# Performance work log

Measured on AMD Instinct MI355X. Metric: run time of the kernel, lower is better.

The kernel has to match this reference:

```python
import jax, jax.numpy as jnp
import numpy as np

L, B, E = 2048, 4, 1024
H = 8
D1 = 2048          # expand_ratio * E, multiple of H
HD = D1 // H       # head dim 256
MAX_L = 2048
EPS = 1e-8


def setup_inputs() -> dict:
    key = jax.random.key(0)
    ks = jax.random.split(key, 9)
    std = 0.02
    return {
        "x": jax.random.normal(ks[0], (L, B, E), jnp.float32),
        "Wu": jax.random.normal(ks[1], (D1, E), jnp.float32) * std,
        "bu": jax.random.normal(ks[2], (D1,), jnp.float32) * std,
        "Wv": jax.random.normal(ks[3], (D1, E), jnp.float32) * std,
        "bv": jax.random.normal(ks[4], (D1,), jnp.float32) * std,
        "Wo": jax.random.normal(ks[5], (E, D1), jnp.float32) * std,
        "bo": jax.random.normal(ks[6], (E,), jnp.float32) * std,
        "zero": jax.random.normal(ks[7], (H, 1), jnp.float32) * 0.1,   # Toeplitz coef, offset 0
        "pos": jax.random.normal(ks[8], (H, MAX_L - 1), jnp.float32) * 0.1,  # offsets 1..n-1
    }


def _simple_rmsnorm(x):
    d = x.shape[-1]
    rms = jnp.linalg.norm(x, axis=-1, keepdims=True) * (d ** -0.5)
    return x / (rms + EPS)


def _toeplitz_causal_fft(v, zero, pos):
    # v: (b, h, n, hd); causal Toeplitz mixing along n via FFT long conv
    n = v.shape[-2]
    coef = jnp.concatenate([zero, pos[:, : n - 1]], axis=-1)  # (h, n)
    m = 2 * n
    cf = jnp.fft.rfft(coef, m, axis=-1)                  # (h, m//2+1)
    vf = jnp.fft.rfft(v, m, axis=-2)                     # (b, h, m//2+1, hd)
    out = jnp.fft.irfft(cf[None, :, :, None] * vf, m, axis=-2)
    return out[:, :, :n, :]


def reference(x, Wu, bu, Wv, bv, Wo, bo, zero, pos):
    # x: (n, b, e) fairseq layout
    n, b, e = x.shape
    shortcut = x
    xn = _simple_rmsnorm(x)                               # pre_norm (SimpleRMSNorm, no params)
    u = jax.nn.silu(jnp.einsum('nbe,de->nbd', xn, Wu) + bu)   # (n,b,d1)
    v = jax.nn.silu(jnp.einsum('nbe,de->nbd', xn, Wv) + bv)   # (n,b,d1)
    # 'n b (h d) -> b h n d'
    vh = v.transpose(1, 0, 2).reshape(b, n, H, HD).transpose(0, 2, 1, 3)
    oh = _toeplitz_causal_fft(vh, zero, pos)              # (b,h,n,hd)
    o = oh.transpose(0, 2, 1, 3).reshape(b, n, D1).transpose(1, 0, 2)  # (n,b,d1)
    o = u * o                                             # gating
    out = jnp.einsum('nbd,ed->nbe', o, Wo) + bo + shortcut
    return out
```

## Files before the change

### kernel.cpp

```cpp
#include <hip/hip_runtime.h>
#include <cstdint>
#include <cstddef>

#define LQ   2048
#define BQ   4
#define EQ   1024
#define HQ   8
#define D1Q  2048
#define HDQ  256
#define NBQ  (LQ*BQ)

typedef __bf16 bf16_t;
typedef __bf16 bf16x8 __attribute__((ext_vector_type(8)));
typedef __bf16 bf16x4 __attribute__((ext_vector_type(4)));
typedef float  f32x4  __attribute__((ext_vector_type(4)));

#define GAS1(p) ((const __attribute__((address_space(1))) void*)(p))
#define LAS3(p) ((__attribute__((address_space(3))) void*)(p))


__global__ __launch_bounds__(256) void convert_kernel(
    const float* __restrict__ Wu, const float* __restrict__ Wv,
    const float* __restrict__ Wo,
    bf16_t* __restrict__ Wub, bf16_t* __restrict__ Wvb,
    bf16_t* __restrict__ Wob)
{
    const size_t i = (size_t)blockIdx.x * 256 + threadIdx.x;
    if (i < (size_t)D1Q * EQ) {
        Wub[i] = (bf16_t)Wu[i];
        Wvb[i] = (bf16_t)Wv[i];
        Wob[i] = (bf16_t)Wo[i];
    }
}

__global__ __launch_bounds__(256) void build_toep_tiles(
    const float* __restrict__ zero, const float* __restrict__ pos,
    bf16_t* __restrict__ Atiles)
{
    const int q = blockIdx.x;
    const int h = blockIdx.y;
    const int doff = (q - 3) * 32;
    const int tid = threadIdx.x;
    bf16_t* dst = Atiles + ((size_t)h * 64 + q) * (128 * 32);
    const int e0 = tid * 16;
    const int r = e0 >> 5;
    const int cbase = e0 & 31;
    bf16_t vals[16];
    #pragma unroll
    for (int j = 0; j < 16; ++j) {
        const int d = doff + r - (cbase + j);
        float v = 0.f;
        if (d == 0) v = zero[h];
        else if (d > 0) v = pos[(size_t)h * (LQ - 1) + d - 1];
        vals[j] = (bf16_t)v;
    }
    *(bf16x8*)(dst + e0)     = *(bf16x8*)(vals);
    *(bf16x8*)(dst + e0 + 8) = *(bf16x8*)(vals + 8);
}

__global__ __launch_bounds__(256) void rmsnorm_kernel(
    const float* __restrict__ x, bf16_t* __restrict__ xn)
{
    const int row = blockIdx.x;
    const int tid = threadIdx.x;
    const float4 v = ((const float4*)(x + (size_t)row * EQ))[tid];
    float ss = v.x*v.x + v.y*v.y + v.z*v.z + v.w*v.w;
    #pragma unroll
    for (int m = 32; m >= 1; m >>= 1) ss += __shfl_xor(ss, m, 64);
    __shared__ float red[4];
    const int wid = tid >> 6, lane = tid & 63;
    if (lane == 0) red[wid] = ss;
    __syncthreads();
    const float tot = red[0] + red[1] + red[2] + red[3];
    const float inv = 1.f / (sqrtf(tot * (1.f / EQ)) + 1e-8f);
    bf16x4 o;
    o[0] = (bf16_t)(v.x * inv); o[1] = (bf16_t)(v.y * inv);
    o[2] = (bf16_t)(v.z * inv); o[3] = (bf16_t)(v.w * inv);
    *(bf16x4*)(xn + (size_t)row * EQ + tid * 4) = o;
}

__global__ __launch_bounds__(256) void transpose_v(
    const bf16_t* __restrict__ V, bf16_t* __restrict__ VT)
{
    __shared__ bf16_t tile[64][65];
    const int bh = blockIdx.z;
    const int b = bh >> 3, h = bh & 7;
    const int s0 = blockIdx.x * 64, hd0 = blockIdx.y * 64;
    const int tid = threadIdx.x;
    #pragma unroll
    for (int p = 0; p < 16; ++p) {
        const int idx = p * 256 + tid;
        const int i = idx >> 6;
        const int j = idx & 63;
        tile[i][j] = V[((size_t)(s0 + i) * BQ + b) * D1Q + h * HDQ + hd0 + j];
    }
    __syncthreads();
    #pragma unroll
    for (int p = 0; p < 16; ++p) {
        const int idx = p * 256 + tid;
        const int i = idx >> 6;
        const int j = idx & 63;
        VT[((size_t)bh * HDQ + hd0 + i) * LQ + s0 + j] = tile[j][i];
    }
}


template<int NREP, int MODE>
__global__ __launch_bounds__(512, 1) void gemm8p(
    const bf16_t* __restrict__ A, const bf16_t* __restrict__ Bm,
    int K, int N,
    const float* __restrict__ bias, const float* __restrict__ res,
    bf16_t* __restrict__ Cb, float* __restrict__ Cf)
{
    constexpr int LB      = NREP / 2;
    constexpr int BSTRIDE = 16384 + NREP * 4096;
    __shared__ alignas(16) char smem[3 * BSTRIDE];

    const int tid  = threadIdx.x;
    const int wid  = tid >> 6;
    const int lane = tid & 63;
    const int frow = lane & 15;
    const int c    = lane >> 4;
    const int m0 = blockIdx.y * 256;
    const int n0 = blockIdx.x * (NREP * 64);
    const int wrm = (wid >> 2) * 128;
    const int wrn = (wid & 3) * (NREP * 16);

    const int Ra = wrm + frow;
    const int ga = (Ra ^ (Ra >> 2)) & 3;
    const int offA = Ra * 64 + ((c ^ ga) << 4);
    const int Rb = wrn + frow;
    const int gb = (Rb ^ (Rb >> 2)) & 3;
    const int offB = 16384 + Rb * 64 + ((c ^ gb) << 4);

    const int sr   = tid >> 2;
    const int slot = tid & 3;
    const int gs   = (sr ^ (sr >> 2)) & 3;
    const size_t lda = (size_t)K * 2;
    const char* srcA  = (const char*)A  + (size_t)(m0 + sr) * lda + ((slot ^ gs) << 4);
    const char* srcA2 = srcA + 128 * lda;
    const char* srcB  = (const char*)Bm + (size_t)(n0 + sr) * lda + ((slot ^ gs) << 4);
    const char* srcB2 = srcB + 128 * lda;

    auto STAGE_A = [&](int buf, int kt) {
        char* d = smem + buf * BSTRIDE + wid * 1024;
        __builtin_amdgcn_global_load_lds(GAS1(srcA  + (size_t)kt * 64), LAS3(d), 16, 0, 0);
        __builtin_amdgcn_global_load_lds(GAS1(srcA2 + (size_t)kt * 64), LAS3(d + 8192), 16, 0, 0);
    };
    auto STAGE_B = [&](int buf, int kt) {
        char* d = smem + buf * BSTRIDE + 16384 + wid * 1024;
        __builtin_amdgcn_global_load_lds(GAS1(srcB  + (size_t)kt * 64), LAS3(d), 16, 0, 0);
        if constexpr (LB == 2)
            __builtin_amdgcn_global_load_lds(GAS1(srcB2 + (size_t)kt * 64), LAS3(d + 8192), 16, 0, 0);
    };

    f32x4 acc[8][NREP];
    #pragma unroll
    for (int i = 0; i < 8; ++i)
        #pragma unroll
        for (int j = 0; j < NREP; ++j) acc[i][j] = (f32x4){0.f, 0.f, 0.f, 0.f};

    const int NT = K >> 5;

    STAGE_A(0, 0); STAGE_B(0, 0);
    STAGE_A(1, 1); STAGE_B(1, 1);
    if constexpr (LB == 2) asm volatile("s_waitcnt vmcnt(4)" ::: "memory");
    else                   asm volatile("s_waitcnt vmcnt(3)" ::: "memory");
    __builtin_amdgcn_s_barrier();

    int buf = 0;
    for (int kq = 0; kq < NT; ++kq) {
        const char* base = smem + buf * BSTRIDE;
        int pbuf = buf + 2; if (pbuf >= 3) pbuf -= 3;
        const bool pf = (kq < NT - 2);

        bf16x8 av[4], bv[NREP];
        #pragma unroll
        for (int i = 0; i < 4; ++i)
            av[i] = *(const bf16x8*)(base + offA + i * 1024);
        #pragma unroll
        for (int i = 0; i < NREP; ++i)
            bv[i] = *(const bf16x8*)(base + offB + i * 1024);
        if (pf) STAGE_A(pbuf, kq + 2);
        __builtin_amdgcn_s_barrier();
        __builtin_amdgcn_s_setprio(1);
        #pragma unroll
        for (int mi = 0; mi < 4; ++mi)
            #pragma unroll
            for (int ni = 0; ni < NREP; ++ni)
                acc[mi][ni] = __builtin_amdgcn_mfma_f32_16x16x32_bf16(
                    av[mi], bv[ni], acc[mi][ni], 0, 0, 0);
        __builtin_amdgcn_s_setprio(0);
        __builtin_amdgcn_sched_barrier(0);
        __builtin_amdgcn_s_barrier();

        #pragma unroll
        for (int i = 0; i < 4; ++i)
            av[i] = *(const bf16x8*)(base + offA + (4 + i) * 1024);
        if (pf) STAGE_B(pbuf, kq + 2);
        __builtin_amdgcn_s_barrier();
        __builtin_amdgcn_s_setprio(1);
        #pragma unroll
        for (int mi = 0; mi < 4; ++mi)
            #pragma unroll
            for (int ni = 0; ni < NREP; ++ni)
                acc[4 + mi][ni] = __builtin_amdgcn_mfma_f32_16x16x32_bf16(
                    av[mi], bv[ni], acc[4 + mi][ni], 0, 0, 0);
        __builtin_amdgcn_s_setprio(0);
        __builtin_amdgcn_sched_barrier(0);

        if (kq < NT - 1) {
            if (kq <= NT - 3) {
                if constexpr (LB == 2) asm volatile("s_waitcnt vmcnt(4)" ::: "memory");
                else                   asm volatile("s_waitcnt vmcnt(3)" ::: "memory");
            } else {
                asm volatile("s_waitcnt vmcnt(0)" ::: "memory");
            }
            __builtin_amdgcn_s_barrier();
        }
        buf = (buf == 2) ? 0 : buf + 1;
    }

    const int fq = (lane >> 4) * 4;
    #pragma unroll
    for (int mi = 0; mi < 8; ++mi) {
        #pragma unroll
        for (int ni = 0; ni < NREP; ++ni) {
            const int gn = n0 + wrn + ni * 16 + frow;
            #pragma unroll
            for (int j = 0; j < 4; ++j) {
                const int gm = m0 + wrm + mi * 16 + fq + j;
                float v = acc[mi][ni][j];
                if constexpr (MODE == 0) {
                    v += bias[gn];
                    v = v / (1.f + __expf(-v));
                    Cb[(size_t)gm * N + gn] = (bf16_t)v;
                } else {
                    v += bias[gn] + res[(size_t)gm * N + gn];
                    Cf[(size_t)gm * N + gn] = v;
                }
            }
        }
    }
}

__global__ __launch_bounds__(256) void gemm_toep(
    const bf16_t* __restrict__ VT, const bf16_t* __restrict__ Atiles,
    const bf16_t* __restrict__ U, bf16_t* __restrict__ O)
{
    constexpr int BM = 128, BN = 128, BK = 32;
    __shared__ alignas(16) bf16_t As[BM * BK];
    __shared__ alignas(16) bf16_t Bs[BN * BK];

    const int bid   = blockIdx.x;
    const int m_blk = 15 - (bid >> 6);
    const int sub   = bid & 63;
    const int bh    = sub >> 1;
    const int n0    = (sub & 1) * BN;
    const int b = bh >> 3, h = bh & 7;
    const int m0 = m_blk * BM;

    const int tid  = threadIdx.x;
    const int wid  = tid >> 6;
    const int lane = tid & 63;
    const int wr = (wid >> 1) * 64;
    const int wc = (wid & 1) * 64;

    f32x4 acc[4][4];
    #pragma unroll
    for (int i = 0; i < 4; ++i)
        #pragma unroll
        for (int j = 0; j < 4; ++j) acc[i][j] = (f32x4){0.f, 0.f, 0.f, 0.f};

    const int off0 = wid * 1024 + lane * 16;
    const int off1 = off0 + 4096;
    const int r0 = off0 >> 6, c0 = off0 & 63;
    const int r1 = off1 >> 6, c1 = off1 & 63;
    const char* Bb = (const char*)(VT + ((size_t)bh * HDQ + n0) * LQ);
    const size_t ldb = (size_t)LQ * 2;
    const char* Ah = (const char*)(Atiles + (size_t)h * 64 * 4096);

    const int frow = lane & 15;
    const int fk   = (lane >> 4) * 8;
    const int nk   = 4 * m_blk + 4;

    for (int kq = 0; kq < nk; ++kq) {
        const int k0 = kq * 32;
        const char* At = Ah + (size_t)((m_blk << 2) + 3 - kq) * 8192;
        __builtin_amdgcn_global_load_lds(GAS1(At + off0),
                                         LAS3((char*)As + wid * 1024), 16, 0, 0);
        __builtin_amdgcn_global_load_lds(GAS1(At + off1),
                                         LAS3((char*)As + 4096 + wid * 1024), 16, 0, 0);
        __builtin_amdgcn_global_load_lds(GAS1(Bb + (size_t)r0 * ldb + (size_t)k0 * 2 + c0),
                                         LAS3((char*)Bs + wid * 1024), 16, 0, 0);
        __builtin_amdgcn_global_load_lds(GAS1(Bb + (size_t)r1 * ldb + (size_t)k0 * 2 + c1),
                                         LAS3((char*)Bs + 4096 + wid * 1024), 16, 0, 0);
        __syncthreads();

        bf16x8 af[4], bfv[4];
        #pragma unroll
        for (int i = 0; i < 4; ++i) {
            af[i]  = *(const bf16x8*)(As + (wr + i * 16 + frow) * BK + fk);
            bfv[i] = *(const bf16x8*)(Bs + (wc + i * 16 + frow) * BK + fk);
        }
        #pragma unroll
        for (int mi = 0; mi < 4; ++mi)
            #pragma unroll
            for (int ni = 0; ni < 4; ++ni)
                acc[mi][ni] = __builtin_amdgcn_mfma_f32_16x16x32_bf16(
                    af[mi], bfv[ni], acc[mi][ni], 0, 0, 0);
        __syncthreads();
    }

    const int fq = (lane >> 4) * 4;
    #pragma unroll
    for (int mi = 0; mi < 4; ++mi) {
        #pragma unroll
        for (int ni = 0; ni < 4; ++ni) {
            const int hd = n0 + wc + ni * 16 + frow;
            #pragma unroll
            for (int j = 0; j < 4; ++j) {
                const int t = m0 + wr + mi * 16 + fq + j;
                const size_t idx = ((size_t)t * BQ + b) * D1Q + h * HDQ + hd;
                const float uval = (float)U[idx];
                O[idx] = (bf16_t)(uval * acc[mi][ni][j]);
            }
        }
    }
}


extern "C" void kernel_launch(void* const* d_in, const int* in_sizes, int n_in,
                              void* d_out, int out_size, void* d_ws, size_t ws_size,
                              hipStream_t stream)
{
    const float* x    = (const float*)d_in[0];
    const float* Wu   = (const float*)d_in[1];
    const float* bu   = (const float*)d_in[2];
    const float* Wv   = (const float*)d_in[3];
    const float* bv   = (const float*)d_in[4];
    const float* Wo   = (const float*)d_in[5];
    const float* bo   = (const float*)d_in[6];
    const float* zero = (const float*)d_in[7];
    const float* pos  = (const float*)d_in[8];
    float* out = (float*)d_out;

    char* ws = (char*)d_ws;
    size_t off = 0;
    auto alloc = [&](size_t bytes) {
        char* p = ws + off;
        off += (bytes + 255) & ~(size_t)255;
        return p;
    };
    bf16_t* xn     = (bf16_t*)alloc((size_t)NBQ * EQ * 2);
    bf16_t* Wub    = (bf16_t*)alloc((size_t)D1Q * EQ * 2);
    bf16_t* Wvb    = (bf16_t*)alloc((size_t)D1Q * EQ * 2);
    bf16_t* Wob    = (bf16_t*)alloc((size_t)EQ * D1Q * 2);
    bf16_t* Atiles = (bf16_t*)alloc((size_t)HQ * 64 * 4096 * 2);
    bf16_t* Ub     = (bf16_t*)alloc((size_t)NBQ * D1Q * 2);
    bf16_t* Vb     = (bf16_t*)alloc((size_t)NBQ * D1Q * 2);
    bf16_t* VTb    = (bf16_t*)alloc((size_t)NBQ * D1Q * 2);
    bf16_t* Ob     = (bf16_t*)alloc((size_t)NBQ * D1Q * 2);

    convert_kernel<<<8192, 256, 0, stream>>>(Wu, Wv, Wo, Wub, Wvb, Wob);
    build_toep_tiles<<<dim3(64, 8), 256, 0, stream>>>(zero, pos, Atiles);
    rmsnorm_kernel<<<NBQ, 256, 0, stream>>>(x, xn);

    dim3 g1(D1Q / 256, NBQ / 256);
    gemm8p<4, 0><<<g1, 512, 0, stream>>>(xn, Wub, EQ, D1Q, bu, nullptr, Ub, nullptr);
    gemm8p<4, 0><<<g1, 512, 0, stream>>>(xn, Wvb, EQ, D1Q, bv, nullptr, Vb, nullptr);

    transpose_v<<<dim3(LQ / 64, HDQ / 64, BQ * HQ), 256, 0, stream>>>(Vb, VTb);

    gemm_toep<<<1024, 256, 0, stream>>>(VTb, Atiles, Ub, Ob);

    dim3 g2(EQ / 128, NBQ / 256);
    gemm8p<2, 2><<<g2, 512, 0, stream>>>(Ob, Wob, D1Q, EQ, bo, x, nullptr, out);
}
```

Measured before the change: 236.5 us.

## Fuse V transpose into GEMM epilogue, batch Toeplitz over B, remap workgroups

```diff
diff --git a/kernel.cpp b/kernel.cpp
--- a/kernel.cpp
+++ b/kernel.cpp
@@ -79,31 +79,6 @@
     *(bf16x4*)(xn + (size_t)row * EQ + tid * 4) = o;
 }
 
-__global__ __launch_bounds__(256) void transpose_v(
-    const bf16_t* __restrict__ V, bf16_t* __restrict__ VT)
-{
-    __shared__ bf16_t tile[64][65];
-    const int bh = blockIdx.z;
-    const int b = bh >> 3, h = bh & 7;
-    const int s0 = blockIdx.x * 64, hd0 = blockIdx.y * 64;
-    const int tid = threadIdx.x;
-    #pragma unroll
-    for (int p = 0; p < 16; ++p) {
-        const int idx = p * 256 + tid;
-        const int i = idx >> 6;
-        const int j = idx & 63;
-        tile[i][j] = V[((size_t)(s0 + i) * BQ + b) * D1Q + h * HDQ + hd0 + j];
-    }
-    __syncthreads();
-    #pragma unroll
-    for (int p = 0; p < 16; ++p) {
-        const int idx = p * 256 + tid;
-        const int i = idx >> 6;
-        const int j = idx & 63;
-        VT[((size_t)bh * HDQ + hd0 + i) * LQ + s0 + j] = tile[j][i];
-    }
-}
-
 
 template<int NREP, int MODE>
 __global__ __launch_bounds__(512, 1) void gemm8p(
@@ -116,13 +91,20 @@
     constexpr int BSTRIDE = 16384 + NREP * 4096;
     __shared__ alignas(16) char smem[3 * BSTRIDE];
 
+    const int nwg   = gridDim.x * gridDim.y;
+    const int bid   = blockIdx.y * gridDim.x + blockIdx.x;
+    const int chunk = nwg >> 3;
+    const int sb    = (bid & 7) * chunk + (bid >> 3);
+    const int bx    = sb % gridDim.x;
+    const int by    = sb / gridDim.x;
+
     const int tid  = threadIdx.x;
     const int wid  = tid >> 6;
     const int lane = tid & 63;
     const int frow = lane & 15;
     const int c    = lane >> 4;
-    const int m0 = blockIdx.y * 256;
-    const int n0 = blockIdx.x * (NREP * 64);
+    const int m0 = by * 256;
+    const int n0 = bx * (NREP * 64);
     const int wrm = (wid >> 2) * 128;
     const int wrn = (wid & 3) * (NREP * 16);
 
@@ -221,7 +203,7 @@
         buf = (buf == 2) ? 0 : buf + 1;
     }
 
-    const int fq = (lane >> 4) * 4;
+    const int fq = c * 4;
     #pragma unroll
     for (int mi = 0; mi < 8; ++mi) {
         #pragma unroll
@@ -235,6 +217,12 @@
                     v += bias[gn];
                     v = v / (1.f + __expf(-v));
                     Cb[(size_t)gm * N + gn] = (bf16_t)v;
+                } else if constexpr (MODE == 1) {
+                    v += bias[gn];
+                    v = v / (1.f + __expf(-v));
+                    const int t = gm >> 2, b2 = gm & 3;
+                    const int hh = gn >> 8, hd = gn & 255;
+                    Cb[(((size_t)hh * 4 + b2) * 256 + hd) * LQ + t] = (bf16_t)v;
                 } else {
                     v += bias[gn] + res[(size_t)gm * N + gn];
                     Cf[(size_t)gm * N + gn] = v;
@@ -244,27 +232,56 @@
     }
 }
 
-__global__ __launch_bounds__(256) void gemm_toep(
+__global__ __launch_bounds__(512, 4) void gemm_toep8p(
     const bf16_t* __restrict__ VT, const bf16_t* __restrict__ Atiles,
     const bf16_t* __restrict__ U, bf16_t* __restrict__ O)
 {
-    constexpr int BM = 128, BN = 128, BK = 32;
-    __shared__ alignas(16) bf16_t As[BM * BK];
-    __shared__ alignas(16) bf16_t Bs[BN * BK];
+    constexpr int BSTRIDE = 24576;
+    __shared__ alignas(16) char smem[3 * BSTRIDE];
 
     const int bid   = blockIdx.x;
-    const int m_blk = 15 - (bid >> 6);
-    const int sub   = bid & 63;
-    const int bh    = sub >> 1;
-    const int n0    = (sub & 1) * BN;
-    const int b = bh >> 3, h = bh & 7;
-    const int m0 = m_blk * BM;
+    const int m_blk = 15 - (bid >> 5);
+    const int sub   = bid & 31;
+    const int h     = sub >> 2;
+    const int n0    = (sub & 3) * 256;
+    const int m0    = m_blk * 128;
 
     const int tid  = threadIdx.x;
     const int wid  = tid >> 6;
     const int lane = tid & 63;
-    const int wr = (wid >> 1) * 64;
-    const int wc = (wid & 1) * 64;
+    const int frow = lane & 15;
+    const int c    = lane >> 4;
+    const int wrm  = (wid >> 2) * 64;
+    const int wrn  = (wid & 3) * 64;
+
+    const int Ra = wrm + frow;
+    const int ga = (Ra ^ (Ra >> 2)) & 3;
+    const int offA = Ra * 64 + ((c ^ ga) << 4);
+    const int Rb = wrn + frow;
+    const int gb = (Rb ^ (Rb >> 2)) & 3;
+    const int offB = 8192 + Rb * 64 + ((c ^ gb) << 4);
+
+    const int sr   = tid >> 2;
+    const int slot = tid & 3;
+    const int gs   = (sr ^ (sr >> 2)) & 3;
+    const int soff = (slot ^ gs) << 4;
+
+    const char* Ah = (const char*)(Atiles + (size_t)h * 64 * 4096);
+    const size_t ldb = (size_t)LQ * 2;
+    const char* srcB  = (const char*)VT + ((size_t)h * 1024 + n0 + sr) * ldb + soff;
+    const char* srcB2 = srcB + 128 * ldb;
+
+    auto STAGE_A = [&](int buf, int kt) {
+        const int q = 4 * m_blk + 3 - kt;
+        const char* s = Ah + (size_t)q * 8192 + (size_t)sr * 64 + soff;
+        __builtin_amdgcn_global_load_lds(GAS1(s),
+                                         LAS3(smem + buf * BSTRIDE + wid * 1024), 16, 0, 0);
+    };
+    auto STAGE_B = [&](int buf, int kt) {
+        char* d = smem + buf * BSTRIDE + 8192 + wid * 1024;
+        __builtin_amdgcn_global_load_lds(GAS1(srcB  + (size_t)kt * 64), LAS3(d), 16, 0, 0);
+        __builtin_amdgcn_global_load_lds(GAS1(srcB2 + (size_t)kt * 64), LAS3(d + 8192), 16, 0, 0);
+    };
 
     f32x4 acc[4][4];
     #pragma unroll
@@ -272,55 +289,72 @@
         #pragma unroll
         for (int j = 0; j < 4; ++j) acc[i][j] = (f32x4){0.f, 0.f, 0.f, 0.f};
 
-    const int off0 = wid * 1024 + lane * 16;
-    const int off1 = off0 + 4096;
-    const int r0 = off0 >> 6, c0 = off0 & 63;
-    const int r1 = off1 >> 6, c1 = off1 & 63;
-    const char* Bb = (const char*)(VT + ((size_t)bh * HDQ + n0) * LQ);
-    const size_t ldb = (size_t)LQ * 2;
-    const char* Ah = (const char*)(Atiles + (size_t)h * 64 * 4096);
-
-    const int frow = lane & 15;
-    const int fk   = (lane >> 4) * 8;
-    const int nk   = 4 * m_blk + 4;
-
-    for (int kq = 0; kq < nk; ++kq) {
-        const int k0 = kq * 32;
-        const char* At = Ah + (size_t)((m_blk << 2) + 3 - kq) * 8192;
-        __builtin_amdgcn_global_load_lds(GAS1(At + off0),
-                                         LAS3((char*)As + wid * 1024), 16, 0, 0);
-        __builtin_amdgcn_global_load_lds(GAS1(At + off1),
-                                         LAS3((char*)As + 4096 + wid * 1024), 16, 0, 0);
-        __builtin_amdgcn_global_load_lds(GAS1(Bb + (size_t)r0 * ldb + (size_t)k0 * 2 + c0),
-                                         LAS3((char*)Bs + wid * 1024), 16, 0, 0);
-        __builtin_amdgcn_global_load_lds(GAS1(Bb + (size_t)r1 * ldb + (size_t)k0 * 2 + c1),
-                                         LAS3((char*)Bs + 4096 + wid * 1024), 16, 0, 0);
-        __syncthreads();
-
-        bf16x8 af[4], bfv[4];
-        #pragma unroll
-        for (int i = 0; i < 4; ++i) {
-            af[i]  = *(const bf16x8*)(As + (wr + i * 16 + frow) * BK + fk);
-            bfv[i] = *(const bf16x8*)(Bs + (wc + i * 16 + frow) * BK + fk);
+    const int NT = 4 * m_blk + 4;
+
+    STAGE_A(0, 0); STAGE_B(0, 0);
+    STAGE_A(1, 1); STAGE_B(1, 1);
+    asm volatile("s_waitcnt vmcnt(3)" ::: "memory");
+    __builtin_amdgcn_s_barrier();
+
+    int buf = 0;
+    for (int kq = 0; kq < NT; ++kq) {
+        const char* base = smem + buf * BSTRIDE;
+        int pbuf = buf + 2; if (pbuf >= 3) pbuf -= 3;
+        const bool pf = (kq < NT - 2);
+
+        bf16x8 av[4], bv[4];
+        #pragma unroll
+        for (int i = 0; i < 4; ++i)
+            av[i] = *(const bf16x8*)(base + offA + i * 1024);
+        #pragma unroll
+        for (int i = 0; i < 2; ++i)
+            bv[i] = *(const bf16x8*)(base + offB + i * 1024);
+        if (pf) STAGE_A(pbuf, kq + 2);
+        __builtin_amdgcn_s_barrier();
+        __builtin_amdgcn_s_setprio(1);
+        #pragma unroll
+        for (int mi = 0; mi < 4; ++mi)
+            #pragma unroll
+            for (int ni = 0; ni < 2; ++ni)
+                acc[mi][ni] = __builtin_amdgcn_mfma_f32_16x16x32_bf16(
+                    av[mi], bv[ni], acc[mi][ni], 0, 0, 0);
+        __builtin_amdgcn_s_setprio(0);
+        __builtin_amdgcn_sched_barrier(0);
+        __builtin_amdgcn_s_barrier();
+
+        #pragma unroll
+        for (int i = 2; i < 4; ++i)
+            bv[i] = *(const bf16x8*)(base + offB + i * 1024);
+        if (pf) STAGE_B(pbuf, kq + 2);
+        __builtin_amdgcn_s_barrier();
+        __builtin_amdgcn_s_setprio(1);
+        #pragma unroll
+        for (int mi = 0; mi < 4; ++mi)
+            #pragma unroll
+            for (int ni = 2; ni < 4; ++ni)
+                acc[mi][ni] = __builtin_amdgcn_mfma_f32_16x16x32_bf16(
+                    av[mi], bv[ni], acc[mi][ni], 0, 0, 0);
+        __builtin_amdgcn_s_setprio(0);
+        __builtin_amdgcn_sched_barrier(0);
+
+        if (kq < NT - 1) {
+            if (kq <= NT - 3) asm volatile("s_waitcnt vmcnt(3)" ::: "memory");
+            else              asm volatile("s_waitcnt vmcnt(0)" ::: "memory");
+            __builtin_amdgcn_s_barrier();
         }
-        #pragma unroll
-        for (int mi = 0; mi < 4; ++mi)
-            #pragma unroll
-            for (int ni = 0; ni < 4; ++ni)
-                acc[mi][ni] = __builtin_amdgcn_mfma_f32_16x16x32_bf16(
-                    af[mi], bfv[ni], acc[mi][ni], 0, 0, 0);
-        __syncthreads();
-    }
-
-    const int fq = (lane >> 4) * 4;
+        buf = (buf == 2) ? 0 : buf + 1;
+    }
+
+    const int fq = c * 4;
     #pragma unroll
     for (int mi = 0; mi < 4; ++mi) {
         #pragma unroll
         for (int ni = 0; ni < 4; ++ni) {
-            const int hd = n0 + wc + ni * 16 + frow;
+            const int nn = n0 + wrn + ni * 16 + frow;
+            const int b  = nn >> 8, hd = nn & 255;
             #pragma unroll
             for (int j = 0; j < 4; ++j) {
-                const int t = m0 + wr + mi * 16 + fq + j;
+                const int t = m0 + wrm + mi * 16 + fq + j;
                 const size_t idx = ((size_t)t * BQ + b) * D1Q + h * HDQ + hd;
                 const float uval = (float)U[idx];
                 O[idx] = (bf16_t)(uval * acc[mi][ni][j]);
@@ -358,7 +392,6 @@
     bf16_t* Wob    = (bf16_t*)alloc((size_t)EQ * D1Q * 2);
     bf16_t* Atiles = (bf16_t*)alloc((size_t)HQ * 64 * 4096 * 2);
     bf16_t* Ub     = (bf16_t*)alloc((size_t)NBQ * D1Q * 2);
-    bf16_t* Vb     = (bf16_t*)alloc((size_t)NBQ * D1Q * 2);
     bf16_t* VTb    = (bf16_t*)alloc((size_t)NBQ * D1Q * 2);
     bf16_t* Ob     = (bf16_t*)alloc((size_t)NBQ * D1Q * 2);
 
@@ -368,11 +401,9 @@
 
     dim3 g1(D1Q / 256, NBQ / 256);
     gemm8p<4, 0><<<g1, 512, 0, stream>>>(xn, Wub, EQ, D1Q, bu, nullptr, Ub, nullptr);
-    gemm8p<4, 0><<<g1, 512, 0, stream>>>(xn, Wvb, EQ, D1Q, bv, nullptr, Vb, nullptr);
-
-    transpose_v<<<dim3(LQ / 64, HDQ / 64, BQ * HQ), 256, 0, stream>>>(Vb, VTb);
-
-    gemm_toep<<<1024, 256, 0, stream>>>(VTb, Atiles, Ub, Ob);
+    gemm8p<4, 1><<<g1, 512, 0, stream>>>(xn, Wvb, EQ, D1Q, bv, nullptr, VTb, nullptr);
+
+    gemm_toep8p<<<512, 512, 0, stream>>>(VTb, Atiles, Ub, Ob);
 
     dim3 g2(EQ / 128, NBQ / 256);
     gemm8p<2, 2><<<g2, 512, 0, stream>>>(Ob, Wob, D1Q, EQ, bo, x, nullptr, out);
```

After: 273.5 us. 15.7% more time.
